# Kernel optimization log

Hardware: AMD Instinct MI355X
Metric: run time of the kernel (lower is better)

The kernel has to match this reference:

```python
import jax, jax.numpy as jnp
import numpy as np

T = 8192  # context/question length (input_shape[2])
D = 128   # feature dim (input_shape[3])


def setup_inputs() -> dict:
    key = jax.random.key(0)
    k1, k2 = jax.random.split(key)
    x = jax.random.normal(k1, (2, 1, T, D), dtype=jnp.float32)
    kernel = jax.random.normal(k2, (3 * D,), dtype=jnp.float32)
    return {"x": x, "kernel": kernel}


def reference(x, kernel):
    context = x[0, 0]   # (T, D)
    question = x[1, 0]  # (T, D)
    w_c, w_q, w_m = kernel[:D], kernel[D:2 * D], kernel[2 * D:]

    # Additive similarity: S[i,j] = c_i.w_c + q_j.w_q + (c_i*q_j).w_m
    # Avoids materializing the (T, T, 3D) tiled/concatenated tensor.
    S = (context @ w_c)[:, None] + (question @ w_q)[None, :] \
        + (context * w_m) @ question.T  # (T, T)

    A = jax.nn.softmax(S, axis=-1)  # row-wise softmax, as tf.nn.softmax on 2D

    # C2Q attention: U_A[i] = sum_j A[i,j] * q_j
    U_A = A @ question  # (T, D)

    # Q2C attention: b = row-max of A, h = sum_i b_i * c_i, tiled over rows
    b = jnp.max(A, axis=1)          # (T,)
    h = b @ context                 # (D,)
    H_A = jnp.broadcast_to(h, (T, D))

    # megamerge: [c, U_A, c*U_A, c*H_A]
    G = jnp.concatenate([context, U_A, context * U_A, context * H_A], axis=-1)
    return G  # (T, 4D)
```

## Files before the change

### kernel.cpp

```cpp
#include <hip/hip_runtime.h>
#include <hip/hip_bf16.h>

#define T 8192
#define D 128
#define NSPLIT 8
#define JLEN (T / NSPLIT)
#define BN 64
#define NITER (JLEN / BN)
#define BM 128
#define LOG2E 1.44269504088896f

typedef _Float16 half4_t __attribute__((ext_vector_type(4)));
typedef _Float16 half8_t __attribute__((ext_vector_type(8)));
typedef float floatx4 __attribute__((ext_vector_type(4)));

__global__ void prep_kernel(const float* __restrict__ x, const float* __restrict__ kern,
                            _Float16* __restrict__ q16, _Float16* __restrict__ qT16,
                            _Float16* __restrict__ cm16) {
    const float* context  = x;
    const float* question = x + (size_t)T * D;
    const float* wm = kern + 2 * D;
    __shared__ __align__(16) _Float16 tile[64][65];
    int bx = blockIdx.x;
    int jt = bx & 127;
    int dt = bx >> 7;
    int j0 = jt * 64, d0 = dt * 64;
    int t = threadIdx.x;
    for (int k = 0; k < 16; ++k) {
        int idx = t + k * 256;
        int jj = idx >> 6, dd = idx & 63;
        int j = j0 + jj, d = d0 + dd;
        float qv = question[(size_t)j * D + d];
        _Float16 qh = (_Float16)qv;
        q16[(size_t)j * D + d] = qh;
        tile[jj][dd] = qh;
        float cv = context[(size_t)j * D + d] * wm[d] * LOG2E;
        cm16[(size_t)j * D + d] = (_Float16)cv;
    }
    __syncthreads();
    for (int k = 0; k < 16; ++k) {
        int idx = t + k * 256;
        int dd = idx >> 6, jj = idx & 63;
        qT16[(size_t)(d0 + dd) * T + (j0 + jj)] = tile[jj][dd];
    }
}

__global__ void qq_kernel(const float* __restrict__ x, const float* __restrict__ kern,
                          float* __restrict__ qq2) {
    const float* question = x + (size_t)T * D;
    const float* wq = kern + D;
    int j = blockIdx.x * 256 + threadIdx.x;
    const float4* qrow = (const float4*)(question + (size_t)j * D);
    const float4* w4 = (const float4*)wq;
    float s = 0.f;
    for (int k = 0; k < D / 4; ++k) {
        float4 a = qrow[k], b = w4[k];
        s += a.x * b.x + a.y * b.y + a.z * b.z + a.w * b.w;
    }
    qq2[j] = s * LOG2E;
}

__global__ __launch_bounds__(256, 2)
void flash_kernel(const _Float16* __restrict__ q16, const _Float16* __restrict__ qT16,
                  const _Float16* __restrict__ cm16, const float* __restrict__ qq2,
                  _Float16* __restrict__ Opart, float* __restrict__ mpart,
                  float* __restrict__ lpart) {
    __shared__ __align__(16) _Float16 Kt[64][144];
    __shared__ __align__(16) _Float16 Vt[128][72];
    __shared__ __align__(16) float qqs[JLEN];

    int bx = blockIdx.x;
    int rb = bx >> 3;
    int sp = bx & 7;
    int tid = threadIdx.x;
    int wave = tid >> 6;
    int lane = tid & 63;
    int quad = lane >> 4;
    int l15 = lane & 15;
    int rbase = rb * BM + wave * 32;

    ((float4*)qqs)[tid] = ((const float4*)(qq2 + (size_t)sp * JLEN))[tid];

    half8_t qfrag[2][4];
    for (int mt = 0; mt < 2; ++mt)
        for (int ks = 0; ks < 4; ++ks)
            qfrag[mt][ks] = *(const half8_t*)(cm16 + (size_t)(rbase + mt * 16 + l15) * D
                                              + ks * 32 + quad * 8);

    floatx4 acc[2][8];
    for (int mt = 0; mt < 2; ++mt)
        for (int nt = 0; nt < 8; ++nt)
            for (int r = 0; r < 4; ++r) acc[mt][nt][r] = 0.f;
    float m_run[2] = {-INFINITY, -INFINITY};
    float l_run[2] = {0.f, 0.f};

    for (int it = 0; it < NITER; ++it) {
        int j0 = sp * JLEN + it * BN;
        for (int k = 0; k < 4; ++k) {
            int idx = tid + k * 256;
            int jr = idx >> 4, c8 = idx & 15;
            *(half8_t*)&Kt[jr][c8 * 8] = *(const half8_t*)(q16 + (size_t)(j0 + jr) * D + c8 * 8);
        }
        for (int k = 0; k < 4; ++k) {
            int idx = tid + k * 256;
            int dr = idx >> 3, c8 = idx & 7;
            *(half8_t*)&Vt[dr][c8 * 8] = *(const half8_t*)(qT16 + (size_t)dr * T + j0 + c8 * 8);
        }
        __syncthreads();

        floatx4 St[2][4];
        for (int mt = 0; mt < 2; ++mt)
            for (int jt = 0; jt < 4; ++jt)
                for (int r = 0; r < 4; ++r) St[mt][jt][r] = 0.f;
        for (int ks = 0; ks < 4; ++ks)
            for (int jt = 0; jt < 4; ++jt) {
                half8_t a = *(const half8_t*)&Kt[jt * 16 + l15][ks * 32 + quad * 8];
                St[0][jt] = __builtin_amdgcn_mfma_f32_16x16x32_f16(a, qfrag[0][ks], St[0][jt], 0, 0, 0);
                St[1][jt] = __builtin_amdgcn_mfma_f32_16x16x32_f16(a, qfrag[1][ks], St[1][jt], 0, 0, 0);
            }

        float4 bias[4];
        for (int jt = 0; jt < 4; ++jt)
            bias[jt] = *(const float4*)&qqs[it * 64 + jt * 16 + quad * 4];
        for (int mt = 0; mt < 2; ++mt) {
            St[mt][0][0] += bias[0].x; St[mt][0][1] += bias[0].y; St[mt][0][2] += bias[0].z; St[mt][0][3] += bias[0].w;
            St[mt][1][0] += bias[1].x; St[mt][1][1] += bias[1].y; St[mt][1][2] += bias[1].z; St[mt][1][3] += bias[1].w;
            St[mt][2][0] += bias[2].x; St[mt][2][1] += bias[2].y; St[mt][2][2] += bias[2].z; St[mt][2][3] += bias[2].w;
            St[mt][3][0] += bias[3].x; St[mt][3][1] += bias[3].y; St[mt][3][2] += bias[3].z; St[mt][3][3] += bias[3].w;
        }

        half4_t apv[2][4];
        float alpha[2];
        for (int mt = 0; mt < 2; ++mt) {
            float mx = St[mt][0][0];
            for (int jt = 0; jt < 4; ++jt)
                for (int r = 0; r < 4; ++r) mx = fmaxf(mx, St[mt][jt][r]);
            mx = fmaxf(mx, __shfl_xor(mx, 16));
            mx = fmaxf(mx, __shfl_xor(mx, 32));
            float mnew = fmaxf(m_run[mt], mx);
            alpha[mt] = __builtin_amdgcn_exp2f(m_run[mt] - mnew);
            m_run[mt] = mnew;
            float ps = 0.f;
            for (int jt = 0; jt < 4; ++jt) {
                float p0 = __builtin_amdgcn_exp2f(St[mt][jt][0] - mnew);
                float p1 = __builtin_amdgcn_exp2f(St[mt][jt][1] - mnew);
                float p2 = __builtin_amdgcn_exp2f(St[mt][jt][2] - mnew);
                float p3 = __builtin_amdgcn_exp2f(St[mt][jt][3] - mnew);
                ps += (p0 + p1) + (p2 + p3);
                apv[mt][jt][0] = (_Float16)p0;
                apv[mt][jt][1] = (_Float16)p1;
                apv[mt][jt][2] = (_Float16)p2;
                apv[mt][jt][3] = (_Float16)p3;
            }
            ps += __shfl_xor(ps, 16);
            ps += __shfl_xor(ps, 32);
            l_run[mt] = l_run[mt] * alpha[mt] + ps;
        }
        for (int mt = 0; mt < 2; ++mt) {
            float aT[4];
            for (int r = 0; r < 4; ++r)
                aT[r] = __shfl(alpha[mt], quad * 4 + r);
            for (int nt = 0; nt < 8; ++nt)
                for (int r = 0; r < 4; ++r) acc[mt][nt][r] *= aT[r];
        }

        for (int jt = 0; jt < 4; ++jt)
            for (int nt = 0; nt < 8; ++nt) {
                half4_t b = *(const half4_t*)&Vt[nt * 16 + l15][jt * 16 + quad * 4];
                acc[0][nt] = __builtin_amdgcn_mfma_f32_16x16x16f16(apv[0][jt], b, acc[0][nt], 0, 0, 0);
                acc[1][nt] = __builtin_amdgcn_mfma_f32_16x16x16f16(apv[1][jt], b, acc[1][nt], 0, 0, 0);
            }
        __syncthreads();
    }

    for (int mt = 0; mt < 2; ++mt) {
        if (quad == 0) {
            int iq = rbase + mt * 16 + l15;
            mpart[(size_t)sp * T + iq] = m_run[mt];
            lpart[(size_t)sp * T + iq] = l_run[mt];
        }
        int i = rbase + mt * 16 + quad * 4;
        for (int nt = 0; nt < 8; ++nt)
            for (int r = 0; r < 4; ++r)
                Opart[((size_t)sp * T + (i + r)) * D + nt * 16 + l15] = (_Float16)acc[mt][nt][r];
    }
}

__global__ void merge_kernel(const _Float16* __restrict__ Opart, const float* __restrict__ mpart,
                             const float* __restrict__ lpart, float* __restrict__ U_A,
                             float* __restrict__ linv) {
    int t = threadIdx.x;
    int i = blockIdx.x * 16 + (t >> 4);
    int c = t & 15;
    float mp[NSPLIT], w[NSPLIT];
    float mstar = -INFINITY;
    for (int sp = 0; sp < NSPLIT; ++sp) {
        mp[sp] = mpart[(size_t)sp * T + i];
        mstar = fmaxf(mstar, mp[sp]);
    }
    float L = 0.f;
    for (int sp = 0; sp < NSPLIT; ++sp) {
        w[sp] = __builtin_amdgcn_exp2f(mp[sp] - mstar);
        L += lpart[(size_t)sp * T + i] * w[sp];
    }
    float invL = 1.0f / L;
    int d0 = c * 8;
    float u[8];
    for (int k = 0; k < 8; ++k) u[k] = 0.f;
    for (int sp = 0; sp < NSPLIT; ++sp) {
        half8_t o = *(const half8_t*)(Opart + ((size_t)sp * T + i) * D + d0);
        for (int k = 0; k < 8; ++k) u[k] += (float)o[k] * w[sp];
    }
    for (int k = 0; k < 8; ++k) U_A[(size_t)i * D + d0 + k] = u[k] * invL;
    if (c == 0) linv[i] = invL;
}

__global__ void hsum_part_kernel(const float* __restrict__ x, const float* __restrict__ linv,
                                 float* __restrict__ hpart) {
    const float* context = x;
    int t = threadIdx.x;
    int d = t & 127, g = t >> 7;
    int i0 = blockIdx.x * 128 + g * 64;
    float s = 0.f;
    for (int k = 0; k < 64; ++k)
        s += context[(size_t)(i0 + k) * D + d] * linv[i0 + k];
    hpart[(size_t)(blockIdx.x * 2 + g) * 128 + d] = s;
}

__global__ void hreduce_kernel(const float* __restrict__ hpart, float* __restrict__ h) {
    int d = threadIdx.x;
    float s = 0.f;
    for (int k = 0; k < 128; ++k) s += hpart[(size_t)k * 128 + d];
    h[d] = s;
}

__global__ void assemble_kernel(const float* __restrict__ x, const float* __restrict__ U_A,
                                const float* __restrict__ h, float* __restrict__ out) {
    const float* context = x;
    int gid = blockIdx.x * 256 + threadIdx.x;
    int base = gid * 4;
    int i = base >> 9;
    int c = base & 511;
    int seg = c >> 7, d = c & 127;
    float4 r;
    if (seg == 0) {
        r = *(const float4*)(context + (size_t)i * D + d);
    } else if (seg == 1) {
        r = *(const float4*)(U_A + (size_t)i * D + d);
    } else if (seg == 2) {
        float4 a = *(const float4*)(context + (size_t)i * D + d);
        float4 b = *(const float4*)(U_A + (size_t)i * D + d);
        r = make_float4(a.x * b.x, a.y * b.y, a.z * b.z, a.w * b.w);
    } else {
        float4 a = *(const float4*)(context + (size_t)i * D + d);
        float4 b = *(const float4*)(h + d);
        r = make_float4(a.x * b.x, a.y * b.y, a.z * b.z, a.w * b.w);
    }
    *(float4*)(out + base) = r;
}

extern "C" void kernel_launch(void* const* d_in, const int* in_sizes, int n_in,
                              void* d_out, int out_size, void* d_ws, size_t ws_size,
                              hipStream_t stream) {
    const float* x = (const float*)d_in[0];
    const float* kern = (const float*)d_in[1];
    float* out = (float*)d_out;

    char* w = (char*)d_ws;
    size_t off = 0;
    _Float16* q16  = (_Float16*)(w + off); off += (size_t)T * D * 2;
    _Float16* qT16 = (_Float16*)(w + off); off += (size_t)T * D * 2;
    _Float16* cm16 = (_Float16*)(w + off); off += (size_t)T * D * 2;
    float* qq2   = (float*)(w + off); off += (size_t)T * 4;
    float* mpart = (float*)(w + off); off += (size_t)NSPLIT * T * 4;
    float* lpart = (float*)(w + off); off += (size_t)NSPLIT * T * 4;
    float* U_A   = (float*)(w + off); off += (size_t)T * D * 4;
    float* linv  = (float*)(w + off); off += (size_t)T * 4;
    float* hpart = (float*)(w + off); off += (size_t)128 * 128 * 4;
    float* h     = (float*)(w + off); off += (size_t)D * 4;

    _Float16* Opart = (_Float16*)d_out;

    prep_kernel<<<256, 256, 0, stream>>>(x, kern, q16, qT16, cm16);
    qq_kernel<<<32, 256, 0, stream>>>(x, kern, qq2);
    flash_kernel<<<512, 256, 0, stream>>>(q16, qT16, cm16, qq2, Opart, mpart, lpart);
    merge_kernel<<<512, 256, 0, stream>>>(Opart, mpart, lpart, U_A, linv);
    hsum_part_kernel<<<64, 256, 0, stream>>>(x, linv, hpart);
    hreduce_kernel<<<1, 128, 0, stream>>>(hpart, h);
    assemble_kernel<<<4096, 256, 0, stream>>>(x, U_A, h, out);
}
```

Before: 141.1 us.

## Fuse prep and qq kernels, prefetch K/V via registers, fold h-sum into merge

Merges the question-bias dot product into the prep kernel, which now processes full 64-row tiles with vectorized loads and a wider transpose tile. The flash kernel now loads the next K/V tile into registers while the current tile is computed, overlapping global loads with MFMA work. The separate h reduction kernels are removed: merge computes context*invL partial sums in shared memory and accumulates them into h with atomics. This cuts three launches and overlaps memory latency, at the cost of extra register pressure and float atomic nondeterminism.

```diff
diff --git a/kernel.cpp b/kernel.cpp
--- a/kernel.cpp
+++ b/kernel.cpp
@@ -16,48 +16,54 @@
 
 __global__ void prep_kernel(const float* __restrict__ x, const float* __restrict__ kern,
                             _Float16* __restrict__ q16, _Float16* __restrict__ qT16,
-                            _Float16* __restrict__ cm16) {
+                            _Float16* __restrict__ cm16, float* __restrict__ qq2,
+                            float* __restrict__ h) {
     const float* context  = x;
     const float* question = x + (size_t)T * D;
+    const float* wq = kern + D;
     const float* wm = kern + 2 * D;
-    __shared__ __align__(16) _Float16 tile[64][65];
-    int bx = blockIdx.x;
-    int jt = bx & 127;
-    int dt = bx >> 7;
-    int j0 = jt * 64, d0 = dt * 64;
+    __shared__ __align__(16) _Float16 tile[64][136];
+    __shared__ float red[64][4];
+    int j0 = blockIdx.x * 64;
     int t = threadIdx.x;
-    for (int k = 0; k < 16; ++k) {
-        int idx = t + k * 256;
-        int jj = idx >> 6, dd = idx & 63;
-        int j = j0 + jj, d = d0 + dd;
-        float qv = question[(size_t)j * D + d];
-        _Float16 qh = (_Float16)qv;
-        q16[(size_t)j * D + d] = qh;
-        tile[jj][dd] = qh;
-        float cv = context[(size_t)j * D + d] * wm[d] * LOG2E;
-        cm16[(size_t)j * D + d] = (_Float16)cv;
-    }
+    int jj = t >> 2, dseg = t & 3;
+    const float4* qrow = (const float4*)(question + (size_t)(j0 + jj) * D + dseg * 32);
+    const float4* crow = (const float4*)(context  + (size_t)(j0 + jj) * D + dseg * 32);
+    const float4* wq4  = (const float4*)(wq + dseg * 32);
+    const float4* wm4  = (const float4*)(wm + dseg * 32);
+    float s = 0.f;
+    for (int c = 0; c < 4; ++c) {
+        float4 q0 = qrow[c * 2], q1 = qrow[c * 2 + 1];
+        float4 w0 = wq4[c * 2], w1 = wq4[c * 2 + 1];
+        s += q0.x * w0.x + q0.y * w0.y + q0.z * w0.z + q0.w * w0.w
+           + q1.x * w1.x + q1.y * w1.y + q1.z * w1.z + q1.w * w1.w;
+        half8_t qh;
+        qh[0] = (_Float16)q0.x; qh[1] = (_Float16)q0.y; qh[2] = (_Float16)q0.z; qh[3] = (_Float16)q0.w;
+        qh[4] = (_Float16)q1.x; qh[5] = (_Float16)q1.y; qh[6] = (_Float16)q1.z; qh[7] = (_Float16)q1.w;
+        *(half8_t*)(q16 + (size_t)(j0 + jj) * D + dseg * 32 + c * 8) = qh;
+        *(half8_t*)&tile[jj][dseg * 32 + c * 8] = qh;
+        float4 c0 = crow[c * 2], c1 = crow[c * 2 + 1];
+        float4 m0 = wm4[c * 2], m1 = wm4[c * 2 + 1];
+        half8_t ch;
+        ch[0] = (_Float16)(c0.x * m0.x * LOG2E); ch[1] = (_Float16)(c0.y * m0.y * LOG2E);
+        ch[2] = (_Float16)(c0.z * m0.z * LOG2E); ch[3] = (_Float16)(c0.w * m0.w * LOG2E);
+        ch[4] = (_Float16)(c1.x * m1.x * LOG2E); ch[5] = (_Float16)(c1.y * m1.y * LOG2E);
+        ch[6] = (_Float16)(c1.z * m1.z * LOG2E); ch[7] = (_Float16)(c1.w * m1.w * LOG2E);
+        *(half8_t*)(cm16 + (size_t)(j0 + jj) * D + dseg * 32 + c * 8) = ch;
+    }
+    red[jj][dseg] = s;
+    if (blockIdx.x == 0 && t < 128) h[t] = 0.f;
     __syncthreads();
-    for (int k = 0; k < 16; ++k) {
-        int idx = t + k * 256;
-        int dd = idx >> 6, jj = idx & 63;
-        qT16[(size_t)(d0 + dd) * T + (j0 + jj)] = tile[jj][dd];
-    }
-}
-
-__global__ void qq_kernel(const float* __restrict__ x, const float* __restrict__ kern,
-                          float* __restrict__ qq2) {
-    const float* question = x + (size_t)T * D;
-    const float* wq = kern + D;
-    int j = blockIdx.x * 256 + threadIdx.x;
-    const float4* qrow = (const float4*)(question + (size_t)j * D);
-    const float4* w4 = (const float4*)wq;
-    float s = 0.f;
-    for (int k = 0; k < D / 4; ++k) {
-        float4 a = qrow[k], b = w4[k];
-        s += a.x * b.x + a.y * b.y + a.z * b.z + a.w * b.w;
-    }
-    qq2[j] = s * LOG2E;
+    if (t < 64)
+        qq2[j0 + t] = (red[t][0] + red[t][1] + red[t][2] + red[t][3]) * LOG2E;
+    for (int k = 0; k < 4; ++k) {
+        int ch = t + k * 256;
+        int d = ch >> 3;
+        int jo = (ch & 7) * 8;
+        half8_t v;
+        for (int s2 = 0; s2 < 8; ++s2) v[s2] = tile[jo + s2][d];
+        *(half8_t*)(qT16 + (size_t)d * T + j0 + jo) = v;
+    }
 }
 
 __global__ __launch_bounds__(256, 2)
@@ -94,19 +100,41 @@
     float m_run[2] = {-INFINITY, -INFINITY};
     float l_run[2] = {0.f, 0.f};
 
-    for (int it = 0; it < NITER; ++it) {
-        int j0 = sp * JLEN + it * BN;
+    half8_t kreg[4], vreg[4];
+    {
+        int j0 = sp * JLEN;
         for (int k = 0; k < 4; ++k) {
             int idx = tid + k * 256;
-            int jr = idx >> 4, c8 = idx & 15;
-            *(half8_t*)&Kt[jr][c8 * 8] = *(const half8_t*)(q16 + (size_t)(j0 + jr) * D + c8 * 8);
+            kreg[k] = *(const half8_t*)(q16 + (size_t)(j0 + (idx >> 4)) * D + (idx & 15) * 8);
         }
         for (int k = 0; k < 4; ++k) {
             int idx = tid + k * 256;
-            int dr = idx >> 3, c8 = idx & 7;
-            *(half8_t*)&Vt[dr][c8 * 8] = *(const half8_t*)(qT16 + (size_t)dr * T + j0 + c8 * 8);
+            vreg[k] = *(const half8_t*)(qT16 + (size_t)(idx >> 3) * T + j0 + (idx & 7) * 8);
+        }
+    }
+
+    for (int it = 0; it < NITER; ++it) {
+        for (int k = 0; k < 4; ++k) {
+            int idx = tid + k * 256;
+            *(half8_t*)&Kt[idx >> 4][(idx & 15) * 8] = kreg[k];
+        }
+        for (int k = 0; k < 4; ++k) {
+            int idx = tid + k * 256;
+            *(half8_t*)&Vt[idx >> 3][(idx & 7) * 8] = vreg[k];
         }
         __syncthreads();
+
+        if (it + 1 < NITER) {
+            int j0n = sp * JLEN + (it + 1) * BN;
+            for (int k = 0; k < 4; ++k) {
+                int idx = tid + k * 256;
+                kreg[k] = *(const half8_t*)(q16 + (size_t)(j0n + (idx >> 4)) * D + (idx & 15) * 8);
+            }
+            for (int k = 0; k < 4; ++k) {
+                int idx = tid + k * 256;
+                vreg[k] = *(const half8_t*)(qT16 + (size_t)(idx >> 3) * T + j0n + (idx & 7) * 8);
+            }
+        }
 
         floatx4 St[2][4];
         for (int mt = 0; mt < 2; ++mt)
@@ -187,8 +215,10 @@
 }
 
 __global__ void merge_kernel(const _Float16* __restrict__ Opart, const float* __restrict__ mpart,
-                             const float* __restrict__ lpart, float* __restrict__ U_A,
-                             float* __restrict__ linv) {
+                             const float* __restrict__ lpart, const float* __restrict__ x,
+                             float* __restrict__ U_A, float* __restrict__ h) {
+    __shared__ float hs[256][8];
+    const float* context = x;
     int t = threadIdx.x;
     int i = blockIdx.x * 16 + (t >> 4);
     int c = t & 15;
@@ -212,26 +242,17 @@
         for (int k = 0; k < 8; ++k) u[k] += (float)o[k] * w[sp];
     }
     for (int k = 0; k < 8; ++k) U_A[(size_t)i * D + d0 + k] = u[k] * invL;
-    if (c == 0) linv[i] = invL;
-}
-
-__global__ void hsum_part_kernel(const float* __restrict__ x, const float* __restrict__ linv,
-                                 float* __restrict__ hpart) {
-    const float* context = x;
-    int t = threadIdx.x;
-    int d = t & 127, g = t >> 7;
-    int i0 = blockIdx.x * 128 + g * 64;
-    float s = 0.f;
-    for (int k = 0; k < 64; ++k)
-        s += context[(size_t)(i0 + k) * D + d] * linv[i0 + k];
-    hpart[(size_t)(blockIdx.x * 2 + g) * 128 + d] = s;
-}
-
-__global__ void hreduce_kernel(const float* __restrict__ hpart, float* __restrict__ h) {
-    int d = threadIdx.x;
-    float s = 0.f;
-    for (int k = 0; k < 128; ++k) s += hpart[(size_t)k * 128 + d];
-    h[d] = s;
+    float4 c0 = *(const float4*)(context + (size_t)i * D + d0);
+    float4 c1 = *(const float4*)(context + (size_t)i * D + d0 + 4);
+    hs[t][0] = c0.x * invL; hs[t][1] = c0.y * invL; hs[t][2] = c0.z * invL; hs[t][3] = c0.w * invL;
+    hs[t][4] = c1.x * invL; hs[t][5] = c1.y * invL; hs[t][6] = c1.z * invL; hs[t][7] = c1.w * invL;
+    __syncthreads();
+    if (t < 128) {
+        int d = t, cc = d >> 3, k = d & 7;
+        float s = 0.f;
+        for (int r = 0; r < 16; ++r) s += hs[r * 16 + cc][k];
+        atomicAdd(&h[d], s);
+    }
 }
 
 __global__ void assemble_kernel(const float* __restrict__ x, const float* __restrict__ U_A,
@@ -275,17 +296,12 @@
     float* mpart = (float*)(w + off); off += (size_t)NSPLIT * T * 4;
     float* lpart = (float*)(w + off); off += (size_t)NSPLIT * T * 4;
     float* U_A   = (float*)(w + off); off += (size_t)T * D * 4;
-    float* linv  = (float*)(w + off); off += (size_t)T * 4;
-    float* hpart = (float*)(w + off); off += (size_t)128 * 128 * 4;
     float* h     = (float*)(w + off); off += (size_t)D * 4;
 
     _Float16* Opart = (_Float16*)d_out;
 
-    prep_kernel<<<256, 256, 0, stream>>>(x, kern, q16, qT16, cm16);
-    qq_kernel<<<32, 256, 0, stream>>>(x, kern, qq2);
+    prep_kernel<<<128, 256, 0, stream>>>(x, kern, q16, qT16, cm16, qq2, h);
     flash_kernel<<<512, 256, 0, stream>>>(q16, qT16, cm16, qq2, Opart, mpart, lpart);
-    merge_kernel<<<512, 256, 0, stream>>>(Opart, mpart, lpart, U_A, linv);
-    hsum_part_kernel<<<64, 256, 0, stream>>>(x, linv, hpart);
-    hreduce_kernel<<<1, 128, 0, stream>>>(hpart, h);
+    merge_kernel<<<512, 256, 0, stream>>>(Opart, mpart, lpart, x, U_A, h);
     assemble_kernel<<<4096, 256, 0, stream>>>(x, U_A, h, out);
 }
```

After: 138.5 us. Within noise of the previous version (-1.8%).

## Double-buffer K/V tiles in flash kernel and fuse qq into vectorized prep

Applied to the files above, without the earlier changes.

The flash kernel now prefetches the next K/V tile into registers while computing on the current one, writing into double-buffered LDS and dropping the trailing barrier. The V load order is permuted and B fragments are read as wider 8-half chunks. The prep kernel is rewritten to process full rows with float4 loads, fold in the qq bias dot product via shuffles, and write the transpose with 8-half stores; merge stores are vectorized. This doubles the flash kernel's LDS footprint and adds register pressure, which may reduce occupancy under the 2-blocks launch bound.

```diff
diff --git a/kernel.cpp b/kernel.cpp
--- a/kernel.cpp
+++ b/kernel.cpp
@@ -16,48 +16,42 @@
 
 __global__ void prep_kernel(const float* __restrict__ x, const float* __restrict__ kern,
                             _Float16* __restrict__ q16, _Float16* __restrict__ qT16,
-                            _Float16* __restrict__ cm16) {
+                            _Float16* __restrict__ cm16, float* __restrict__ qq2) {
     const float* context  = x;
     const float* question = x + (size_t)T * D;
+    const float* wq = kern + D;
     const float* wm = kern + 2 * D;
-    __shared__ __align__(16) _Float16 tile[64][65];
-    int bx = blockIdx.x;
-    int jt = bx & 127;
-    int dt = bx >> 7;
-    int j0 = jt * 64, d0 = dt * 64;
+    __shared__ __align__(16) _Float16 tile[32][136];
+    int j0 = blockIdx.x * 32;
     int t = threadIdx.x;
-    for (int k = 0; k < 16; ++k) {
-        int idx = t + k * 256;
-        int jj = idx >> 6, dd = idx & 63;
-        int j = j0 + jj, d = d0 + dd;
-        float qv = question[(size_t)j * D + d];
-        _Float16 qh = (_Float16)qv;
-        q16[(size_t)j * D + d] = qh;
-        tile[jj][dd] = qh;
-        float cv = context[(size_t)j * D + d] * wm[d] * LOG2E;
-        cm16[(size_t)j * D + d] = (_Float16)cv;
+    int c4 = t & 31;
+    int rsub = t >> 5;
+    float4 wqv = ((const float4*)wq)[c4];
+    float4 wmv = ((const float4*)wm)[c4];
+    for (int p = 0; p < 4; ++p) {
+        int row = p * 8 + rsub;
+        float4 q = ((const float4*)(question + (size_t)(j0 + row) * D))[c4];
+        float4 c = ((const float4*)(context  + (size_t)(j0 + row) * D))[c4];
+        half4_t qh;
+        qh[0] = (_Float16)q.x; qh[1] = (_Float16)q.y; qh[2] = (_Float16)q.z; qh[3] = (_Float16)q.w;
+        *(half4_t*)(q16 + (size_t)(j0 + row) * D + c4 * 4) = qh;
+        *(half4_t*)&tile[row][c4 * 4] = qh;
+        half4_t ch;
+        ch[0] = (_Float16)(c.x * wmv.x * LOG2E); ch[1] = (_Float16)(c.y * wmv.y * LOG2E);
+        ch[2] = (_Float16)(c.z * wmv.z * LOG2E); ch[3] = (_Float16)(c.w * wmv.w * LOG2E);
+        *(half4_t*)(cm16 + (size_t)(j0 + row) * D + c4 * 4) = ch;
+        float s = q.x * wqv.x + q.y * wqv.y + q.z * wqv.z + q.w * wqv.w;
+        for (int dx = 1; dx <= 16; dx <<= 1) s += __shfl_xor(s, dx);
+        if (c4 == 0) qq2[j0 + row] = s * LOG2E;
     }
     __syncthreads();
-    for (int k = 0; k < 16; ++k) {
-        int idx = t + k * 256;
-        int dd = idx >> 6, jj = idx & 63;
-        qT16[(size_t)(d0 + dd) * T + (j0 + jj)] = tile[jj][dd];
-    }
-}
-
-__global__ void qq_kernel(const float* __restrict__ x, const float* __restrict__ kern,
-                          float* __restrict__ qq2) {
-    const float* question = x + (size_t)T * D;
-    const float* wq = kern + D;
-    int j = blockIdx.x * 256 + threadIdx.x;
-    const float4* qrow = (const float4*)(question + (size_t)j * D);
-    const float4* w4 = (const float4*)wq;
-    float s = 0.f;
-    for (int k = 0; k < D / 4; ++k) {
-        float4 a = qrow[k], b = w4[k];
-        s += a.x * b.x + a.y * b.y + a.z * b.z + a.w * b.w;
-    }
-    qq2[j] = s * LOG2E;
+    for (int p = 0; p < 2; ++p) {
+        int chunk = t + p * 256;
+        int d = chunk >> 2, jo = (chunk & 3) * 8;
+        half8_t v;
+        for (int s2 = 0; s2 < 8; ++s2) v[s2] = tile[jo + s2][d];
+        *(half8_t*)(qT16 + (size_t)d * T + j0 + jo) = v;
+    }
 }
 
 __global__ __launch_bounds__(256, 2)
@@ -65,8 +59,8 @@
                   const _Float16* __restrict__ cm16, const float* __restrict__ qq2,
                   _Float16* __restrict__ Opart, float* __restrict__ mpart,
                   float* __restrict__ lpart) {
-    __shared__ __align__(16) _Float16 Kt[64][144];
-    __shared__ __align__(16) _Float16 Vt[128][72];
+    __shared__ __align__(16) _Float16 Kt[2][64][144];
+    __shared__ __align__(16) _Float16 Vt[2][128][72];
     __shared__ __align__(16) float qqs[JLEN];
 
     int bx = blockIdx.x;
@@ -94,19 +88,44 @@
     float m_run[2] = {-INFINITY, -INFINITY};
     float l_run[2] = {0.f, 0.f};
 
-    for (int it = 0; it < NITER; ++it) {
-        int j0 = sp * JLEN + it * BN;
+    half8_t kreg[4];
+    half4_t vlo[4], vhi[4];
+
+    {
+        int j0 = sp * JLEN;
         for (int k = 0; k < 4; ++k) {
             int idx = tid + k * 256;
-            int jr = idx >> 4, c8 = idx & 15;
-            *(half8_t*)&Kt[jr][c8 * 8] = *(const half8_t*)(q16 + (size_t)(j0 + jr) * D + c8 * 8);
-        }
+            kreg[k] = *(const half8_t*)(q16 + (size_t)(j0 + (idx >> 4)) * D + (idx & 15) * 8);
+            int dr = idx >> 3, c8 = idx & 7;
+            int base = j0 + (c8 >> 2) * 32 + (c8 & 3) * 4;
+            vlo[k] = *(const half4_t*)(qT16 + (size_t)dr * T + base);
+            vhi[k] = *(const half4_t*)(qT16 + (size_t)dr * T + base + 16);
+        }
+    }
+
+    for (int it = 0; it < NITER; ++it) {
+        int b = it & 1;
         for (int k = 0; k < 4; ++k) {
             int idx = tid + k * 256;
-            int dr = idx >> 3, c8 = idx & 7;
-            *(half8_t*)&Vt[dr][c8 * 8] = *(const half8_t*)(qT16 + (size_t)dr * T + j0 + c8 * 8);
+            *(half8_t*)&Kt[b][idx >> 4][(idx & 15) * 8] = kreg[k];
+            half8_t v;
+            v[0] = vlo[k][0]; v[1] = vlo[k][1]; v[2] = vlo[k][2]; v[3] = vlo[k][3];
+            v[4] = vhi[k][0]; v[5] = vhi[k][1]; v[6] = vhi[k][2]; v[7] = vhi[k][3];
+            *(half8_t*)&Vt[b][idx >> 3][(idx & 7) * 8] = v;
         }
         __syncthreads();
+
+        if (it + 1 < NITER) {
+            int j0n = sp * JLEN + (it + 1) * BN;
+            for (int k = 0; k < 4; ++k) {
+                int idx = tid + k * 256;
+                kreg[k] = *(const half8_t*)(q16 + (size_t)(j0n + (idx >> 4)) * D + (idx & 15) * 8);
+                int dr = idx >> 3, c8 = idx & 7;
+                int base = j0n + (c8 >> 2) * 32 + (c8 & 3) * 4;
+                vlo[k] = *(const half4_t*)(qT16 + (size_t)dr * T + base);
+                vhi[k] = *(const half4_t*)(qT16 + (size_t)dr * T + base + 16);
+            }
+        }
 
         floatx4 St[2][4];
         for (int mt = 0; mt < 2; ++mt)
@@ -114,7 +133,7 @@
                 for (int r = 0; r < 4; ++r) St[mt][jt][r] = 0.f;
         for (int ks = 0; ks < 4; ++ks)
             for (int jt = 0; jt < 4; ++jt) {
-                half8_t a = *(const half8_t*)&Kt[jt * 16 + l15][ks * 32 + quad * 8];
+                half8_t a = *(const half8_t*)&Kt[b][jt * 16 + l15][ks * 32 + quad * 8];
                 St[0][jt] = __builtin_amdgcn_mfma_f32_16x16x32_f16(a, qfrag[0][ks], St[0][jt], 0, 0, 0);
                 St[1][jt] = __builtin_amdgcn_mfma_f32_16x16x32_f16(a, qfrag[1][ks], St[1][jt], 0, 0, 0);
             }
@@ -164,13 +183,21 @@
                 for (int r = 0; r < 4; ++r) acc[mt][nt][r] *= aT[r];
         }
 
-        for (int jt = 0; jt < 4; ++jt)
-            for (int nt = 0; nt < 8; ++nt) {
-                half4_t b = *(const half4_t*)&Vt[nt * 16 + l15][jt * 16 + quad * 4];
-                acc[0][nt] = __builtin_amdgcn_mfma_f32_16x16x16f16(apv[0][jt], b, acc[0][nt], 0, 0, 0);
-                acc[1][nt] = __builtin_amdgcn_mfma_f32_16x16x16f16(apv[1][jt], b, acc[1][nt], 0, 0, 0);
+        for (int pr = 0; pr < 2; ++pr) {
+            half8_t bb[8];
+            for (int nt = 0; nt < 8; ++nt)
+                bb[nt] = *(const half8_t*)&Vt[b][nt * 16 + l15][pr * 32 + quad * 8];
+            for (int h = 0; h < 2; ++h) {
+                int jt = pr * 2 + h;
+                for (int nt = 0; nt < 8; ++nt) {
+                    half4_t bv;
+                    bv[0] = bb[nt][h * 4 + 0]; bv[1] = bb[nt][h * 4 + 1];
+                    bv[2] = bb[nt][h * 4 + 2]; bv[3] = bb[nt][h * 4 + 3];
+                    acc[0][nt] = __builtin_amdgcn_mfma_f32_16x16x16f16(apv[0][jt], bv, acc[0][nt], 0, 0, 0);
+                    acc[1][nt] = __builtin_amdgcn_mfma_f32_16x16x16f16(apv[1][jt], bv, acc[1][nt], 0, 0, 0);
+                }
             }
-        __syncthreads();
+        }
     }
 
     for (int mt = 0; mt < 2; ++mt) {
@@ -211,7 +238,10 @@
         half8_t o = *(const half8_t*)(Opart + ((size_t)sp * T + i) * D + d0);
         for (int k = 0; k < 8; ++k) u[k] += (float)o[k] * w[sp];
     }
-    for (int k = 0; k < 8; ++k) U_A[(size_t)i * D + d0 + k] = u[k] * invL;
+    float4 s0 = make_float4(u[0] * invL, u[1] * invL, u[2] * invL, u[3] * invL);
+    float4 s1 = make_float4(u[4] * invL, u[5] * invL, u[6] * invL, u[7] * invL);
+    *(float4*)(U_A + (size_t)i * D + d0) = s0;
+    *(float4*)(U_A + (size_t)i * D + d0 + 4) = s1;
     if (c == 0) linv[i] = invL;
 }
 
@@ -281,8 +311,7 @@
 
     _Float16* Opart = (_Float16*)d_out;
 
-    prep_kernel<<<256, 256, 0, stream>>>(x, kern, q16, qT16, cm16);
-    qq_kernel<<<32, 256, 0, stream>>>(x, kern, qq2);
+    prep_kernel<<<256, 256, 0, stream>>>(x, kern, q16, qT16, cm16, qq2);
     flash_kernel<<<512, 256, 0, stream>>>(q16, qT16, cm16, qq2, Opart, mpart, lpart);
     merge_kernel<<<512, 256, 0, stream>>>(Opart, mpart, lpart, U_A, linv);
     hsum_part_kernel<<<64, 256, 0, stream>>>(x, linv, hpart);
```

Result: faster. 136.2 us (-3.5%).
